# Performance work log

Measured on AMD Instinct MI355X. Metric: run time of the kernel, lower is better.

Reference implementation:

```python
import jax, jax.numpy as jnp
import numpy as np

B, L, C = 64, 16384, 64
NEG_SLOPE = 0.3  # keras LeakyReLU default


def setup_inputs() -> dict:
    key = jax.random.key(0)
    ks = jax.random.split(key, 8)
    inp = {
        "xatt": jax.random.normal(ks[0], (B, L, C), dtype=jnp.float32),
        "xsaut": jax.random.normal(ks[1], (B, L, C), dtype=jnp.float32),
        # Conv1D(1, kernel=1): weight [C_in, C_out], bias [C_out]
        "W_act": jax.random.normal(ks[2], (C, 1), dtype=jnp.float32) * (1.0 / np.sqrt(C)),
        "b_act": jnp.zeros((1,), dtype=jnp.float32),
        "W_saut": jax.random.normal(ks[3], (C, 1), dtype=jnp.float32) * (1.0 / np.sqrt(C)),
        "b_saut": jnp.zeros((1,), dtype=jnp.float32),
        "W2": jax.random.normal(ks[4], (1, 1), dtype=jnp.float32),
        "b2": jnp.zeros((1,), dtype=jnp.float32),
    }
    return inp


def reference(xatt, xsaut, W_act, b_act, W_saut, b_saut, W2, b2):
    # 1x1 Conv1D == per-position linear projection C -> 1
    xa = jnp.einsum("blc,co->blo", xatt, W_act) + b_act      # [B, L, 1]
    xs = jnp.einsum("blc,co->blo", xsaut, W_saut) + b_saut   # [B, L, 1]
    h = xa + xs
    h = jnp.where(h >= 0, h, NEG_SLOPE * h)                   # LeakyReLU(0.3)
    g = jax.nn.sigmoid(h * W2[0, 0] + b2[0])                  # Conv2 is 1->1 channel
    return g * xs                                             # note: gates the projected skip
```

## Files before the change

kernel.cpp:

```cpp
#include <hip/hip_runtime.h>
#include <math.h>


#define NEG_SLOPE 0.3f
#define C_DIM 64

__global__ __launch_bounds__(256) void attn_gate_kernel(
    const float* __restrict__ xatt,
    const float* __restrict__ xsaut,
    const float* __restrict__ W_act,
    const float* __restrict__ b_act,
    const float* __restrict__ W_saut,
    const float* __restrict__ b_saut,
    const float* __restrict__ W2,
    const float* __restrict__ b2,
    float* __restrict__ out,
    int npos)
{
    const int lane16  = threadIdx.x & 15;
    const int group   = (blockIdx.x * blockDim.x + threadIdx.x) >> 4;
    const int ngroups = (gridDim.x * blockDim.x) >> 4;

    const float4 wa = ((const float4*)W_act)[lane16];
    const float4 ws = ((const float4*)W_saut)[lane16];
    const float  ba = b_act[0];
    const float  bs = b_saut[0];
    const float  w2 = W2[0];
    const float  c2 = b2[0];

    const float4* __restrict__ a4 = (const float4*)xatt;
    const float4* __restrict__ s4 = (const float4*)xsaut;

    for (int pos = group; pos < npos; pos += ngroups) {
        const long base = (long)pos * (C_DIM / 4) + lane16;
        const float4 a = a4[base];
        const float4 s = s4[base];

        float pa = a.x * wa.x + a.y * wa.y + a.z * wa.z + a.w * wa.w;
        float ps = s.x * ws.x + s.y * ws.y + s.z * ws.z + s.w * ws.w;

        #pragma unroll
        for (int off = 8; off > 0; off >>= 1) {
            pa += __shfl_xor(pa, off, 16);
            ps += __shfl_xor(ps, off, 16);
        }

        if (lane16 == 0) {
            const float xa = pa + ba;
            const float xs = ps + bs;
            float h = xa + xs;
            h = (h >= 0.0f) ? h : NEG_SLOPE * h;
            const float z = h * w2 + c2;
            const float g = 1.0f / (1.0f + __expf(-z));
            out[pos] = g * xs;
        }
    }
}

extern "C" void kernel_launch(void* const* d_in, const int* in_sizes, int n_in,
                              void* d_out, int out_size, void* d_ws, size_t ws_size,
                              hipStream_t stream) {
    const float* xatt   = (const float*)d_in[0];
    const float* xsaut  = (const float*)d_in[1];
    const float* W_act  = (const float*)d_in[2];
    const float* b_act  = (const float*)d_in[3];
    const float* W_saut = (const float*)d_in[4];
    const float* b_saut = (const float*)d_in[5];
    const float* W2     = (const float*)d_in[6];
    const float* b2     = (const float*)d_in[7];
    float* out = (float*)d_out;

    const int npos = out_size;

    const int blocks = 4096;
    attn_gate_kernel<<<blocks, 256, 0, stream>>>(
        xatt, xsaut, W_act, b_act, W_saut, b_saut, W2, b2, out, npos);
}
```

Baseline: 513.8 us.

## Use four threads per position with one-shot grid and shorter shuffle reduction

```diff
diff --git a/kernel.cpp b/kernel.cpp
--- a/kernel.cpp
+++ b/kernel.cpp
@@ -3,7 +3,14 @@
 
 
 #define NEG_SLOPE 0.3f
-#define C_DIM 64
+
+__device__ __forceinline__ float dot4(const float4 a, const float4 w, float acc) {
+    acc = fmaf(a.x, w.x, acc);
+    acc = fmaf(a.y, w.y, acc);
+    acc = fmaf(a.z, w.z, acc);
+    acc = fmaf(a.w, w.w, acc);
+    return acc;
+}
 
 __global__ __launch_bounds__(256) void attn_gate_kernel(
     const float* __restrict__ xatt,
@@ -17,43 +24,55 @@
     float* __restrict__ out,
     int npos)
 {
-    const int lane16  = threadIdx.x & 15;
-    const int group   = (blockIdx.x * blockDim.x + threadIdx.x) >> 4;
-    const int ngroups = (gridDim.x * blockDim.x) >> 4;
+    const int tid = blockIdx.x * blockDim.x + threadIdx.x;
+    const int pos = tid >> 2;
+    const int q   = tid & 3;
+    if (pos >= npos) return;
 
-    const float4 wa = ((const float4*)W_act)[lane16];
-    const float4 ws = ((const float4*)W_saut)[lane16];
-    const float  ba = b_act[0];
-    const float  bs = b_saut[0];
-    const float  w2 = W2[0];
-    const float  c2 = b2[0];
+    const float ba = b_act[0];
+    const float bs = b_saut[0];
+    const float w2 = W2[0];
+    const float c2 = b2[0];
 
     const float4* __restrict__ a4 = (const float4*)xatt;
     const float4* __restrict__ s4 = (const float4*)xsaut;
+    const long base = (long)pos * 16 + q;
 
-    for (int pos = group; pos < npos; pos += ngroups) {
-        const long base = (long)pos * (C_DIM / 4) + lane16;
-        const float4 a = a4[base];
-        const float4 s = s4[base];
+    const float4 a0 = a4[base +  0];
+    const float4 a1 = a4[base +  4];
+    const float4 a2 = a4[base +  8];
+    const float4 a3 = a4[base + 12];
+    const float4 s0 = s4[base +  0];
+    const float4 s1 = s4[base +  4];
+    const float4 s2 = s4[base +  8];
+    const float4 s3 = s4[base + 12];
 
-        float pa = a.x * wa.x + a.y * wa.y + a.z * wa.z + a.w * wa.w;
-        float ps = s.x * ws.x + s.y * ws.y + s.z * ws.z + s.w * ws.w;
+    const float4* __restrict__ wA = (const float4*)W_act;
+    const float4* __restrict__ wS = (const float4*)W_saut;
+    const float4 wa0 = wA[q +  0];
+    const float4 wa1 = wA[q +  4];
+    const float4 wa2 = wA[q +  8];
+    const float4 wa3 = wA[q + 12];
+    const float4 ws0 = wS[q +  0];
+    const float4 ws1 = wS[q +  4];
+    const float4 ws2 = wS[q +  8];
+    const float4 ws3 = wS[q + 12];
 
-        #pragma unroll
-        for (int off = 8; off > 0; off >>= 1) {
-            pa += __shfl_xor(pa, off, 16);
-            ps += __shfl_xor(ps, off, 16);
-        }
+    float pa = dot4(a3, wa3, dot4(a2, wa2, dot4(a1, wa1, dot4(a0, wa0, 0.0f))));
+    float ps = dot4(s3, ws3, dot4(s2, ws2, dot4(s1, ws1, dot4(s0, ws0, 0.0f))));
 
-        if (lane16 == 0) {
-            const float xa = pa + ba;
-            const float xs = ps + bs;
-            float h = xa + xs;
-            h = (h >= 0.0f) ? h : NEG_SLOPE * h;
-            const float z = h * w2 + c2;
-            const float g = 1.0f / (1.0f + __expf(-z));
-            out[pos] = g * xs;
-        }
+    pa += __shfl_xor(pa, 1, 4);
+    pa += __shfl_xor(pa, 2, 4);
+    ps += __shfl_xor(ps, 1, 4);
+    ps += __shfl_xor(ps, 2, 4);
+
+    if (q == 0) {
+        const float xs = ps + bs;
+        float h = (pa + ba) + xs;
+        h = (h >= 0.0f) ? h : NEG_SLOPE * h;
+        const float z = fmaf(h, w2, c2);
+        const float g = 1.0f / (1.0f + __expf(-z));
+        out[pos] = g * xs;
     }
 }
 
@@ -72,7 +91,8 @@
 
     const int npos = out_size;
 
-    const int blocks = 4096;
-    attn_gate_kernel<<<blocks, 256, 0, stream>>>(
+    const int threads = 256;
+    const int blocks  = (int)(((long)npos * 4 + threads - 1) / threads);
+    attn_gate_kernel<<<blocks, threads, 0, stream>>>(
         xatt, xsaut, W_act, b_act, W_saut, b_saut, W2, b2, out, npos);
 }
```

Result: no change. 512.9 us (-0.2%).
